# Optimization experiments

Measured on AMD Instinct MI355X. Metric: run time of the kernel, lower is better.

## Reference

```python
import jax, jax.numpy as jnp
import numpy as np

D_MODEL = 2048
NUM_HEADS = 16
D_K = D_MODEL // NUM_HEADS
ROPE_THETA = 10000.0
B, S = 2, 2048


def setup_inputs() -> dict:
    key = jax.random.key(0)
    ks = jax.random.split(key, 5)
    std = 1.0 / np.sqrt(D_MODEL)
    return {
        "x": jax.random.normal(ks[0], (B, S, D_MODEL), jnp.float32),
        "wq": jax.random.normal(ks[1], (D_MODEL, D_MODEL), jnp.float32) * std,
        "wk": jax.random.normal(ks[2], (D_MODEL, D_MODEL), jnp.float32) * std,
        "wv": jax.random.normal(ks[3], (D_MODEL, D_MODEL), jnp.float32) * std,
        "wo": jax.random.normal(ks[4], (D_MODEL, D_MODEL), jnp.float32) * std,
        "token_positions": jnp.arange(S, dtype=jnp.int32),
    }


def _rope(x, positions):
    # x: [b, h, s, d_k]; positions: [s]
    inv_freq = 1.0 / (ROPE_THETA ** (jnp.arange(0, D_K, 2, dtype=jnp.float32) / D_K))
    freqs = positions.astype(jnp.float32)[:, None] * inv_freq[None, :]  # [s, d_k/2]
    cos, sin = jnp.cos(freqs), jnp.sin(freqs)
    x_even, x_odd = x[..., ::2], x[..., 1::2]
    out_even = x_even * cos - x_odd * sin
    out_odd = x_even * sin + x_odd * cos
    # re-interleave even/odd lanes
    return jnp.stack([out_even, out_odd], axis=-1).reshape(x.shape)


def reference(x, wq, wk, wv, wo, token_positions):
    b, s, _ = x.shape
    # projections: weight is [out, in] as in torch Linear-style einsum
    q = jnp.einsum("bsd,ed->bse", x, wq)
    k = jnp.einsum("bsd,ed->bse", x, wk)
    v = jnp.einsum("bsd,ed->bse", x, wv)
    # split heads: b s (h d) -> b h s d
    def split(t):
        return t.reshape(b, s, NUM_HEADS, D_K).transpose(0, 2, 1, 3)
    q, k, v = split(q), split(k), split(v)
    q = _rope(q, token_positions)
    k = _rope(k, token_positions)
    scores = jnp.einsum("bhmd,bhnd->bhmn", q, k) / jnp.sqrt(jnp.float32(D_K))
    causal = jnp.tril(jnp.ones((s, s), dtype=bool))
    scores = jnp.where(causal[None, None], scores, -jnp.inf)
    attn = jax.nn.softmax(scores, axis=-1)
    out = jnp.einsum("bhmn,bhnd->bhmd", attn, v)
    out = out.transpose(0, 2, 1, 3).reshape(b, s, D_MODEL)
    return jnp.einsum("em,bsm->bse", wo, out)
```

## Files before the change

### kernel.cpp

```cpp
#include <hip/hip_runtime.h>

#define S_LEN 2048
#define DM 2048
#define NH 16
#define DK 128
#define BB 2
#define BH (BB*NH)
#define GK 2048

typedef float f32x4 __attribute__((ext_vector_type(4)));
typedef __bf16 bf16x8 __attribute__((ext_vector_type(8)));
typedef unsigned int u32;

#define AS1 __attribute__((address_space(1)))
#define AS3 __attribute__((address_space(3)))

__device__ inline void gload16(const void* g, void* l){
  __builtin_amdgcn_global_load_lds((AS1 const u32*)g, (AS3 u32*)l, 16, 0, 0);
}

__device__ inline ushort f2bf(float f){
  unsigned u = __float_as_uint(f);
  u = (u + 0x7FFFu + ((u >> 16) & 1u)) >> 16;
  return (ushort)u;
}

__global__ void k_f32_to_bf16(const float* __restrict__ in, ushort* __restrict__ out, int n4){
  int i = blockIdx.x * blockDim.x + threadIdx.x;
  if (i >= n4) return;
  float4 v = reinterpret_cast<const float4*>(in)[i];
  ushort4 o;
  o.x = f2bf(v.x); o.y = f2bf(v.y); o.z = f2bf(v.z); o.w = f2bf(v.w);
  reinterpret_cast<ushort4*>(out)[i] = o;
}

__global__ void k_w4(const float* __restrict__ wq, const float* __restrict__ wk,
                     const float* __restrict__ wv, const float* __restrict__ wo4,
                     ushort* __restrict__ dqkv, ushort* __restrict__ dwo){
  int i = blockIdx.x * 256 + threadIdx.x;
  int sel = i >> 20;
  int off = i & ((1 << 20) - 1);
  const float* s = (sel == 0) ? wq : (sel == 1) ? wk : (sel == 2) ? wv : wo4;
  ushort* d = (sel < 3) ? (dqkv + (size_t)sel * DM * DM) : dwo;
  float4 v = reinterpret_cast<const float4*>(s)[off];
  ushort4 o;
  o.x = f2bf(v.x); o.y = f2bf(v.y); o.z = f2bf(v.z); o.w = f2bf(v.w);
  reinterpret_cast<ushort4*>(d)[off] = o;
}

__global__ void k_rope_table(const int* __restrict__ pos, float2* __restrict__ cs){
  int idx = blockIdx.x * 256 + threadIdx.x;
  if (idx >= S_LEN * 64) return;
  int s = idx >> 6, i = idx & 63;
  float inv = expf(-0.14391156831212787f * (float)i);
  float f = (float)pos[s] * inv;
  cs[idx] = make_float2(cosf(f), sinf(f));
}

#define SBAR() do{ __builtin_amdgcn_s_barrier(); __builtin_amdgcn_sched_barrier(0); }while(0)
#define VMC(n) asm volatile("s_waitcnt vmcnt(" #n ")" ::: "memory")

#define STG(slot, srcp, tks, khh) do{ \
  const ushort* _s = (srcp) + (tks)*64 + (khh)*32; \
  gload16(_s,                    lds + (slot)*8192 + wid*512); \
  gload16(_s + (size_t)128*GK,   lds + (slot)*8192 + 4096 + wid*512); \
}while(0)

#define RD_A(slot, mh) do{ \
  af[0] = *reinterpret_cast<const bf16x8*>(ldsc + (slot)*16384 + wm*8192 + ((mh)*4+0)*1024 + frA); \
  af[1] = *reinterpret_cast<const bf16x8*>(ldsc + (slot)*16384 + wm*8192 + ((mh)*4+1)*1024 + frA); \
  af[2] = *reinterpret_cast<const bf16x8*>(ldsc + (slot)*16384 + wm*8192 + ((mh)*4+2)*1024 + frA); \
  af[3] = *reinterpret_cast<const bf16x8*>(ldsc + (slot)*16384 + wm*8192 + ((mh)*4+3)*1024 + frA); \
}while(0)

#define RD_B(slot) do{ \
  bfr[0] = *reinterpret_cast<const bf16x8*>(ldsc + (slot)*16384 + wn*4096 + 0*1024 + frA); \
  bfr[1] = *reinterpret_cast<const bf16x8*>(ldsc + (slot)*16384 + wn*4096 + 1*1024 + frA); \
  bfr[2] = *reinterpret_cast<const bf16x8*>(ldsc + (slot)*16384 + wn*4096 + 2*1024 + frA); \
  bfr[3] = *reinterpret_cast<const bf16x8*>(ldsc + (slot)*16384 + wn*4096 + 3*1024 + frA); \
}while(0)

#define MM(mh) do{ \
  __builtin_amdgcn_s_setprio(1); \
  _Pragma("unroll") \
  for (int mf2 = 0; mf2 < 4; mf2++) \
    _Pragma("unroll") \
    for (int nf = 0; nf < 4; nf++) \
      acc[(mh)*4+mf2][nf] = __builtin_amdgcn_mfma_f32_16x16x32_bf16(af[mf2], bfr[nf], acc[(mh)*4+mf2][nf], 0, 0, 0); \
  __builtin_amdgcn_s_setprio(0); \
}while(0)

__launch_bounds__(512, 2)
__global__ void k_gemm_qk(const ushort* __restrict__ A, const ushort* __restrict__ Bt,
                          const float2* __restrict__ cs,
                          ushort* __restrict__ Qh, ushort* __restrict__ Kh){
  __shared__ short lds[65536];
  const int tid = threadIdx.x, lane = tid & 63, wid = tid >> 6;
  const int wm = wid >> 2, wn = wid & 3;
  const int fr = lane & 15, fq = lane >> 4;

  const int bid = blockIdx.x;
  const int b2 = (bid & 7) * 32 + (bid >> 3);
  const int by = b2 >> 4, bx = b2 & 15;

  const int rbase = wid * 16 + (lane >> 2);
  const int kup = ((lane & 3) ^ ((lane >> 3) & 3)) * 8;
  const ushort* pa = A  + (size_t)(by * 256 + rbase) * GK + kup;
  const ushort* pb = Bt + (size_t)(bx * 256 + rbase) * GK + kup;

  const char* ldsc = (const char*)lds;
  const int frA = fr * 64 + ((fq * 16) ^ (((fr >> 1) & 3) << 4));

  f32x4 acc[8][4] = {};
  bf16x8 af[4], bfr[4];

  STG(0, pa, 0, 0); STG(1, pb, 0, 0); STG(2, pa, 0, 1); STG(3, pb, 0, 1);
  STG(4, pa, 1, 0); STG(5, pb, 1, 0);
  VMC(8);
  SBAR();

  #pragma unroll 1
  for (int it = 0; it < 16; ++it){
    const int tb  = 2 * it + 1;
    const int tn  = (2 * it + 2 < 32) ? 2 * it + 2 : 31;
    const int tn1 = (2 * it + 3 < 32) ? 2 * it + 3 : 31;
    RD_A(0, 0); RD_B(1); STG(6, pa, tb, 1);           SBAR(); MM(0); SBAR();
    RD_A(0, 1);          STG(7, pb, tb, 1);  VMC(6);  SBAR(); MM(1); SBAR();
    RD_A(2, 0); RD_B(3); STG(0, pa, tn, 0);           SBAR(); MM(0); SBAR();
    RD_A(2, 1);          STG(1, pb, tn, 0);  VMC(6);  SBAR(); MM(1); SBAR();
    RD_A(4, 0); RD_B(5); STG(2, pa, tn, 1);           SBAR(); MM(0); SBAR();
    RD_A(4, 1);          STG(3, pb, tn, 1);  VMC(6);  SBAR(); MM(1); SBAR();
    RD_A(6, 0); RD_B(7); STG(4, pa, tn1, 0);          SBAR(); MM(0); SBAR();
    RD_A(6, 1);          STG(5, pb, tn1, 0); VMC(6);  SBAR(); MM(1); SBAR();
  }

  const int rowb = by * 256 + wm * 128 + fq * 4;
  ushort* dst = (bx < 8) ? Qh : Kh;
  #pragma unroll
  for (int mf = 0; mf < 8; mf++)
    #pragma unroll
    for (int nf = 0; nf < 4; nf++){
      int col = bx * 256 + wn * 64 + nf * 16 + fr;
      int cg = col & 2047;
      int hh = cg >> 7, dd = cg & 127, jj = (cg >> 1) & 63;
      #pragma unroll
      for (int i = 0; i < 4; i++){
        int row = rowb + mf * 16 + i;
        int s = row & (S_LEN - 1), bb = row >> 11;
        float2 c2 = cs[s * 64 + jj];
        float v = acc[mf][nf][i];
        float p = __shfl_xor(v, 1);
        float o = (fr & 1) ? fmaf(p, c2.y, v * c2.x) : fmaf(v, c2.x, -p * c2.y);
        dst[((size_t)(bb * NH + hh) * S_LEN + s) * DK + dd] = f2bf(o);
      }
    }
}

#define WSTG_A(si, tks, khh) do{ \
  const ushort* _s = pa + (tks)*64 + (khh)*32; \
  gload16(_s,                  lds + (si)*8192 + wid*512); \
  gload16(_s + (size_t)128*GK, lds + (si)*8192 + 4096 + wid*512); \
}while(0)
#define WSTG_B(si, tks, khh) do{ \
  const ushort* _s = pb + (tks)*64 + (khh)*32; \
  gload16(_s, lds + 32768 + (si)*4096 + wid*512); \
}while(0)
#define WRD_A(si, mhf) do{ \
  af[0] = *reinterpret_cast<const bf16x8*>(ldsc + (si)*16384 + wm*4096 + ((mhf)*2+0)*1024 + frA); \
  af[1] = *reinterpret_cast<const bf16x8*>(ldsc + (si)*16384 + wm*4096 + ((mhf)*2+1)*1024 + frA); \
}while(0)
#define WRD_B(si) do{ \
  bfr[0] = *reinterpret_cast<const bf16x8*>(ldsc + 65536 + (si)*8192 + wn*4096 + 0*1024 + frA); \
  bfr[1] = *reinterpret_cast<const bf16x8*>(ldsc + 65536 + (si)*8192 + wn*4096 + 1*1024 + frA); \
  bfr[2] = *reinterpret_cast<const bf16x8*>(ldsc + 65536 + (si)*8192 + wn*4096 + 2*1024 + frA); \
  bfr[3] = *reinterpret_cast<const bf16x8*>(ldsc + 65536 + (si)*8192 + wn*4096 + 3*1024 + frA); \
}while(0)
#define WMM(mhf) do{ \
  __builtin_amdgcn_s_setprio(1); \
  _Pragma("unroll") \
  for (int k2 = 0; k2 < 2; k2++) \
    _Pragma("unroll") \
    for (int nf = 0; nf < 4; nf++) \
      acc[(mhf)*2+k2][nf] = __builtin_amdgcn_mfma_f32_16x16x32_bf16(af[k2], bfr[nf], acc[(mhf)*2+k2][nf], 0, 0, 0); \
  __builtin_amdgcn_s_setprio(0); \
}while(0)

#define WBODY() \
  WSTG_A(0, 0, 0); WSTG_B(0, 0, 0); WSTG_A(1, 0, 1); WSTG_B(1, 0, 1); \
  WSTG_A(2, 1, 0); WSTG_B(2, 1, 0); \
  VMC(6); \
  SBAR(); \
  _Pragma("unroll 1") \
  for (int it = 0; it < 16; ++it){ \
    const int tb  = 2 * it + 1; \
    const int tn  = (2 * it + 2 < 32) ? 2 * it + 2 : 31; \
    const int tn1 = (2 * it + 3 < 32) ? 2 * it + 3 : 31; \
    WRD_A(0, 0); WRD_B(0); WSTG_A(3, tb, 1);            SBAR(); WMM(0); SBAR(); \
    WRD_A(0, 1);           WSTG_B(3, tb, 1);  VMC(6);   SBAR(); WMM(1); SBAR(); \
    WRD_A(1, 0); WRD_B(1); WSTG_A(0, tn, 0);            SBAR(); WMM(0); SBAR(); \
    WRD_A(1, 1);           WSTG_B(0, tn, 0);  VMC(6);   SBAR(); WMM(1); SBAR(); \
    WRD_A(2, 0); WRD_B(2); WSTG_A(1, tn, 1);            SBAR(); WMM(0); SBAR(); \
    WRD_A(2, 1);           WSTG_B(1, tn, 1);  VMC(6);   SBAR(); WMM(1); SBAR(); \
    WRD_A(3, 0); WRD_B(3); WSTG_A(2, tn1, 0);           SBAR(); WMM(0); SBAR(); \
    WRD_A(3, 1);           WSTG_B(2, tn1, 0); VMC(6);   SBAR(); WMM(1); SBAR(); \
  }

__launch_bounds__(512, 2)
__global__ void k_gemm_v(const ushort* __restrict__ A, const ushort* __restrict__ Bt,
                         ushort* __restrict__ Vt){
  __shared__ short lds[49152];
  const int tid = threadIdx.x, lane = tid & 63, wid = tid >> 6;
  const int wm = wid >> 1, wn = wid & 1;
  const int fr = lane & 15, fq = lane >> 4;

  const int bid = blockIdx.x;
  const int b2 = (bid & 7) * 32 + (bid >> 3);
  const int by = b2 >> 4, bx = b2 & 15;

  const int rbase = wid * 16 + (lane >> 2);
  const int kup = ((lane & 3) ^ ((lane >> 3) & 3)) * 8;
  const ushort* pa = A  + (size_t)(by * 256 + rbase) * GK + kup;
  const ushort* pb = Bt + (size_t)(bx * 128 + rbase) * GK + kup;

  const char* ldsc = (const char*)lds;
  const int frA = fr * 64 + ((fq * 16) ^ (((fr >> 1) & 3) << 4));

  f32x4 acc[4][4] = {};
  bf16x8 af[2], bfr[4];

  WBODY();

  const int rowb = by * 256 + wm * 64 + fq * 4;
  #pragma unroll
  for (int mf = 0; mf < 4; mf++){
    int row0 = rowb + mf * 16;
    int s0 = row0 & (S_LEN - 1), bb = row0 >> 11;
    #pragma unroll
    for (int nf = 0; nf < 4; nf++){
      int col = bx * 128 + wn * 64 + nf * 16 + fr;
      int hh = col >> 7, dd = col & 127;
      ushort4 o;
      o.x = f2bf(acc[mf][nf][0]); o.y = f2bf(acc[mf][nf][1]);
      o.z = f2bf(acc[mf][nf][2]); o.w = f2bf(acc[mf][nf][3]);
      *reinterpret_cast<ushort4*>(&Vt[((size_t)(bb * NH + hh) * DK + dd) * S_LEN + s0]) = o;
    }
  }
}

__launch_bounds__(512, 2)
__global__ void k_gemm_wo(const ushort* __restrict__ A, const ushort* __restrict__ Bt,
                          float* __restrict__ C){
  __shared__ short lds[49152];
  const int tid = threadIdx.x, lane = tid & 63, wid = tid >> 6;
  const int wm = wid >> 1, wn = wid & 1;
  const int fr = lane & 15, fq = lane >> 4;

  const int bid = blockIdx.x;
  const int b2 = (bid & 7) * 32 + (bid >> 3);
  const int by = b2 >> 4, bx = b2 & 15;

  const int rbase = wid * 16 + (lane >> 2);
  const int kup = ((lane & 3) ^ ((lane >> 3) & 3)) * 8;
  const ushort* pa = A  + (size_t)(by * 256 + rbase) * GK + kup;
  const ushort* pb = Bt + (size_t)(bx * 128 + rbase) * GK + kup;

  const char* ldsc = (const char*)lds;
  const int frA = fr * 64 + ((fq * 16) ^ (((fr >> 1) & 3) << 4));

  f32x4 acc[4][4] = {};
  bf16x8 af[2], bfr[4];

  WBODY();

  const int orow = by * 256 + wm * 64 + fq * 4;
  const int ocol = bx * 128 + wn * 64 + fr;
  #pragma unroll
  for (int mf = 0; mf < 4; mf++)
    #pragma unroll
    for (int nf = 0; nf < 4; nf++)
      #pragma unroll
      for (int i = 0; i < 4; i++)
        C[(size_t)(orow + mf * 16 + i) * DM + ocol + nf * 16] = acc[mf][nf][i];
}

__launch_bounds__(512)
__global__ void k_attn(const ushort* __restrict__ Q, const ushort* __restrict__ K,
                       const ushort* __restrict__ Vt, ushort* __restrict__ O){
  __shared__ short Kt[2][64 * 128];
  __shared__ short Vl[2][128 * 64];
  __shared__ short Pl[8][16 * 64];
  const int tid = threadIdx.x, lane = tid & 63, wid = tid >> 6;
  const int bid = blockIdx.x;
  const int pid = bid >> 5;
  const int bh = bid & 31;
  const int b = bh >> 4, h = bh & 15;
  const int fr = lane & 15, fq = lane >> 4;
  const int swz = (fr & 7) << 4;

  const ushort* kb = K  + (size_t)bh * S_LEN * DK;
  const ushort* vb = Vt + (size_t)bh * DK * S_LEN;
  char* PlB = (char*)Pl + wid * 2048;
  const float scale = 0.08838834764831845f;
  ushort* ob = O + (size_t)b * S_LEN * DM;

  int kro[2], kco[2], vro[2], vco[2];
  #pragma unroll
  for (int jj = 0; jj < 2; jj++){
    int ins = wid * 2 + jj;
    kro[jj] = ins * 4 + (lane >> 4);
    kco[jj] = 8 * ((lane & 15) ^ (kro[jj] & 7));
    vro[jj] = ins * 8 + (lane >> 3);
    vco[jj] = 8 * ((lane & 7) ^ (vro[jj] & 7));
  }

  #pragma unroll 1
  for (int half = 0; half < 2; half++){
    const int j = half ? pid : 15 - pid;
    const int qr = j * 128 + wid * 16;
    const int nt = 2 * j + 2;

    bf16x8 qf[4];
    #pragma unroll
    for (int c = 0; c < 4; c++)
      qf[c] = *reinterpret_cast<const bf16x8*>(
          Q + ((size_t)bh * S_LEN + qr + fr) * DK + c * 32 + fq * 8);

    float mi[4], li[4];
    #pragma unroll
    for (int i = 0; i < 4; i++){ mi[i] = -1e30f; li[i] = 0.f; }
    f32x4 accO[8] = {};

    __syncthreads();
    #pragma unroll
    for (int jj = 0; jj < 2; jj++){
      int ins = wid * 2 + jj;
      gload16(kb + (size_t)kro[jj] * DK + kco[jj],      (char*)Kt + ins * 1024);
      gload16(vb + (size_t)vro[jj] * S_LEN + vco[jj],   (char*)Vl + ins * 1024);
    }
    __syncthreads();

    #pragma unroll 1
    for (int kt = 0; kt < nt; kt++){
      const int k0 = kt * 64;
      const int cur = kt & 1;
      if (kt + 1 < nt){
        const int k1 = k0 + 64;
        #pragma unroll
        for (int jj = 0; jj < 2; jj++){
          int ins = wid * 2 + jj;
          gload16(kb + (size_t)(k1 + kro[jj]) * DK + kco[jj],  (char*)Kt + (cur ^ 1) * 16384 + ins * 1024);
          gload16(vb + (size_t)vro[jj] * S_LEN + k1 + vco[jj], (char*)Vl + (cur ^ 1) * 16384 + ins * 1024);
        }
      }
      const char* KtB = (const char*)Kt + cur * 16384;
      const char* VlB = (const char*)Vl + cur * 16384;

      f32x4 sc[4] = {};
      #pragma unroll
      for (int c = 0; c < 4; c++){
        bf16x8 kf[4];
        #pragma unroll
        for (int ch = 0; ch < 4; ch++)
          kf[ch] = *reinterpret_cast<const bf16x8*>(
              KtB + (ch * 16 + fr) * 256 + ((c * 64 + fq * 16) ^ swz));
        #pragma unroll
        for (int ch = 0; ch < 4; ch++)
          sc[ch] = __builtin_amdgcn_mfma_f32_16x16x32_bf16(qf[c], kf[ch], sc[ch], 0, 0, 0);
      }

      const bool needmask = (k0 + 63 > qr);
      #pragma unroll
      for (int ch = 0; ch < 4; ch++)
        #pragma unroll
        for (int i = 0; i < 4; i++){
          float v = sc[ch][i] * scale;
          if (needmask && (k0 + ch * 16 + fr > qr + fq * 4 + i)) v = -1e30f;
          sc[ch][i] = v;
        }
      f32x4 mx;
      #pragma unroll
      for (int i = 0; i < 4; i++)
        mx[i] = fmaxf(fmaxf(sc[0][i], sc[1][i]), fmaxf(sc[2][i], sc[3][i]));
      #pragma unroll
      for (int off = 1; off < 16; off <<= 1)
        #pragma unroll
        for (int i = 0; i < 4; i++) mx[i] = fmaxf(mx[i], __shfl_xor(mx[i], off));
      float scl[4];
      #pragma unroll
      for (int i = 0; i < 4; i++){
        float mn = fmaxf(mi[i], mx[i]);
        scl[i] = __expf(mi[i] - mn);
        mi[i] = mn;
      }
      #pragma unroll
      for (int ch = 0; ch < 4; ch++)
        #pragma unroll
        for (int i = 0; i < 4; i++) sc[ch][i] = __expf(sc[ch][i] - mi[i]);
      f32x4 rs;
      #pragma unroll
      for (int i = 0; i < 4; i++)
        rs[i] = (sc[0][i] + sc[1][i]) + (sc[2][i] + sc[3][i]);
      #pragma unroll
      for (int off = 1; off < 16; off <<= 1)
        #pragma unroll
        for (int i = 0; i < 4; i++) rs[i] += __shfl_xor(rs[i], off);
      #pragma unroll
      for (int i = 0; i < 4; i++) li[i] = li[i] * scl[i] + rs[i];
      #pragma unroll
      for (int dt = 0; dt < 8; dt++)
        #pragma unroll
        for (int i = 0; i < 4; i++) accO[dt][i] *= scl[i];

      #pragma unroll
      for (int ch = 0; ch < 4; ch++)
        #pragma unroll
        for (int i = 0; i < 4; i++){
          int q = fq * 4 + i;
          int off = q * 128 + ((ch * 32 + fr * 2) ^ ((q & 7) << 4));
          *reinterpret_cast<short*>(PlB + off) = (short)f2bf(sc[ch][i]);
        }
      bf16x8 pf[2];
      #pragma unroll
      for (int c2 = 0; c2 < 2; c2++)
        pf[c2] = *reinterpret_cast<const bf16x8*>(
            PlB + fr * 128 + ((c2 * 64 + fq * 16) ^ swz));

      #pragma unroll
      for (int dt = 0; dt < 8; dt++)
        #pragma unroll
        for (int c2 = 0; c2 < 2; c2++){
          bf16x8 vf = *reinterpret_cast<const bf16x8*>(
              VlB + (dt * 16 + fr) * 128 + ((c2 * 64 + fq * 16) ^ swz));
          accO[dt] = __builtin_amdgcn_mfma_f32_16x16x32_bf16(pf[c2], vf, accO[dt], 0, 0, 0);
        }
      __syncthreads();
    }

    float inv[4];
    #pragma unroll
    for (int i = 0; i < 4; i++) inv[i] = 1.f / li[i];
    #pragma unroll
    for (int dt = 0; dt < 8; dt++)
      #pragma unroll
      for (int i = 0; i < 4; i++){
        int row = qr + fq * 4 + i;
        ob[(size_t)row * DM + h * DK + dt * 16 + fr] = f2bf(accO[dt][i] * inv[i]);
      }
  }
}

extern "C" void kernel_launch(void* const* d_in, const int* in_sizes, int n_in,
                              void* d_out, int out_size, void* d_ws, size_t ws_size,
                              hipStream_t stream){
  const float* x  = (const float*)d_in[0];
  const float* wq = (const float*)d_in[1];
  const float* wk = (const float*)d_in[2];
  const float* wv = (const float*)d_in[3];
  const float* wo = (const float*)d_in[4];
  const int* pos  = (const int*)d_in[5];
  float* out = (float*)d_out;

  char* ws = (char*)d_ws;
  ushort* xb   = (ushort*)(ws);
  ushort* Ob   = xb;
  ushort* wqkv = (ushort*)(ws + 16777216);
  ushort* Qh   = (ushort*)(ws + 41943040);
  ushort* Kh   = (ushort*)(ws + 58720256);
  ushort* Vt   = (ushort*)(ws + 75497472);
  float2* cs   = (float2*)(ws + 92274688);
  ushort* wob  = (ushort*)(ws + 93323264);

  const int M = BB * S_LEN;

  k_rope_table<<<(S_LEN * 64) / 256, 256, 0, stream>>>(pos, cs);
  k_f32_to_bf16<<<(M * DM / 4) / 256, 256, 0, stream>>>(x, xb, M * DM / 4);
  k_w4<<<4 * (DM * DM / 4) / 256, 256, 0, stream>>>(wq, wk, wv, wo, wqkv, wob);

  k_gemm_qk<<<256, 512, 0, stream>>>(xb, wqkv, cs, Qh, Kh);
  k_gemm_v<<<256, 512, 0, stream>>>(xb, wqkv + (size_t)2 * DM * DM, Vt);

  k_attn<<<256, 512, 0, stream>>>(Qh, Kh, Vt, Ob);

  k_gemm_wo<<<256, 512, 0, stream>>>(Ob, wob, out);
}
```

Before: 282.3 us.

## Have each attention wave process 32 query rows to reuse K/V fragments

The attention kernel drops from 8 waves to 4 waves per block, and each wave now handles two 16-row query sub-tiles. K and V fragments read from LDS are reused across both sub-tiles, which halves LDS read traffic per MFMA. Each thread issues twice as many async global-to-LDS loads, and the P staging buffer is resized with a padded 160-byte row stride. The cost is higher register pressure (two sets of accumulators and softmax state per wave) and fewer waves per block to hide latency.

```diff
diff --git a/kernel.cpp b/kernel.cpp
--- a/kernel.cpp
+++ b/kernel.cpp
@@ -283,12 +283,12 @@
         C[(size_t)(orow + mf * 16 + i) * DM + ocol + nf * 16] = acc[mf][nf][i];
 }
 
-__launch_bounds__(512)
+__launch_bounds__(256)
 __global__ void k_attn(const ushort* __restrict__ Q, const ushort* __restrict__ K,
                        const ushort* __restrict__ Vt, ushort* __restrict__ O){
   __shared__ short Kt[2][64 * 128];
   __shared__ short Vl[2][128 * 64];
-  __shared__ short Pl[8][16 * 64];
+  __shared__ short Pl[4][32 * 80];
   const int tid = threadIdx.x, lane = tid & 63, wid = tid >> 6;
   const int bid = blockIdx.x;
   const int pid = bid >> 5;
@@ -299,14 +299,14 @@
 
   const ushort* kb = K  + (size_t)bh * S_LEN * DK;
   const ushort* vb = Vt + (size_t)bh * DK * S_LEN;
-  char* PlB = (char*)Pl + wid * 2048;
+  char* PlB = (char*)Pl + wid * 5120;
   const float scale = 0.08838834764831845f;
   ushort* ob = O + (size_t)b * S_LEN * DM;
 
-  int kro[2], kco[2], vro[2], vco[2];
+  int kro[4], kco[4], vro[4], vco[4];
   #pragma unroll
-  for (int jj = 0; jj < 2; jj++){
-    int ins = wid * 2 + jj;
+  for (int jj = 0; jj < 4; jj++){
+    int ins = wid * 4 + jj;
     kro[jj] = ins * 4 + (lane >> 4);
     kco[jj] = 8 * ((lane & 15) ^ (kro[jj] & 7));
     vro[jj] = ins * 8 + (lane >> 3);
@@ -316,26 +316,33 @@
   #pragma unroll 1
   for (int half = 0; half < 2; half++){
     const int j = half ? pid : 15 - pid;
-    const int qr = j * 128 + wid * 16;
+    const int qr = j * 128 + wid * 32;
     const int nt = 2 * j + 2;
 
-    bf16x8 qf[4];
+    bf16x8 qf[2][4];
     #pragma unroll
-    for (int c = 0; c < 4; c++)
-      qf[c] = *reinterpret_cast<const bf16x8*>(
-          Q + ((size_t)bh * S_LEN + qr + fr) * DK + c * 32 + fq * 8);
-
-    float mi[4], li[4];
+    for (int m = 0; m < 2; m++)
+      #pragma unroll
+      for (int c = 0; c < 4; c++)
+        qf[m][c] = *reinterpret_cast<const bf16x8*>(
+            Q + ((size_t)bh * S_LEN + qr + m * 16 + fr) * DK + c * 32 + fq * 8);
+
+    float mi[2][4], li[2][4];
     #pragma unroll
-    for (int i = 0; i < 4; i++){ mi[i] = -1e30f; li[i] = 0.f; }
-    f32x4 accO[8] = {};
+    for (int m = 0; m < 2; m++)
+      #pragma unroll
+      for (int i = 0; i < 4; i++){ mi[m][i] = -1e30f; li[m][i] = 0.f; }
+    f32x4 accO[2][8] = {};
 
     __syncthreads();
-    #pragma unroll
-    for (int jj = 0; jj < 2; jj++){
-      int ins = wid * 2 + jj;
-      gload16(kb + (size_t)kro[jj] * DK + kco[jj],      (char*)Kt + ins * 1024);
-      gload16(vb + (size_t)vro[jj] * S_LEN + vco[jj],   (char*)Vl + ins * 1024);
+    {
+      char* kd = (char*)Kt + (wid * 4) * 1024;
+      char* vd = (char*)Vl + (wid * 4) * 1024;
+      #pragma unroll
+      for (int jj = 0; jj < 4; jj++){
+        gload16(kb + (size_t)kro[jj] * DK + kco[jj],      kd + jj * 1024);
+        gload16(vb + (size_t)vro[jj] * S_LEN + vco[jj],   vd + jj * 1024);
+      }
     }
     __syncthreads();
 
@@ -345,17 +352,18 @@
       const int cur = kt & 1;
       if (kt + 1 < nt){
         const int k1 = k0 + 64;
-        #pragma unroll
-        for (int jj = 0; jj < 2; jj++){
-          int ins = wid * 2 + jj;
-          gload16(kb + (size_t)(k1 + kro[jj]) * DK + kco[jj],  (char*)Kt + (cur ^ 1) * 16384 + ins * 1024);
-          gload16(vb + (size_t)vro[jj] * S_LEN + k1 + vco[jj], (char*)Vl + (cur ^ 1) * 16384 + ins * 1024);
+        char* kd = (char*)Kt + (cur ^ 1) * 16384 + (wid * 4) * 1024;
+        char* vd = (char*)Vl + (cur ^ 1) * 16384 + (wid * 4) * 1024;
+        #pragma unroll
+        for (int jj = 0; jj < 4; jj++){
+          gload16(kb + (size_t)(k1 + kro[jj]) * DK + kco[jj],    kd + jj * 1024);
+          gload16(vb + (size_t)vro[jj] * S_LEN + k1 + vco[jj],   vd + jj * 1024);
         }
       }
       const char* KtB = (const char*)Kt + cur * 16384;
       const char* VlB = (const char*)Vl + cur * 16384;
 
-      f32x4 sc[4] = {};
+      f32x4 sc[2][4] = {};
       #pragma unroll
       for (int c = 0; c < 4; c++){
         bf16x8 kf[4];
@@ -364,66 +372,75 @@
           kf[ch] = *reinterpret_cast<const bf16x8*>(
               KtB + (ch * 16 + fr) * 256 + ((c * 64 + fq * 16) ^ swz));
         #pragma unroll
+        for (int ch = 0; ch < 4; ch++){
+          sc[0][ch] = __builtin_amdgcn_mfma_f32_16x16x32_bf16(qf[0][c], kf[ch], sc[0][ch], 0, 0, 0);
+          sc[1][ch] = __builtin_amdgcn_mfma_f32_16x16x32_bf16(qf[1][c], kf[ch], sc[1][ch], 0, 0, 0);
+        }
+      }
+
+      #pragma unroll
+      for (int m = 0; m < 2; m++){
+        const int qb = qr + m * 16;
+        const bool needmask = (k0 + 63 > qb);
+        #pragma unroll
         for (int ch = 0; ch < 4; ch++)
-          sc[ch] = __builtin_amdgcn_mfma_f32_16x16x32_bf16(qf[c], kf[ch], sc[ch], 0, 0, 0);
+          #pragma unroll
+          for (int i = 0; i < 4; i++){
+            float v = sc[m][ch][i] * scale;
+            if (needmask && (k0 + ch * 16 + fr > qb + fq * 4 + i)) v = -1e30f;
+            sc[m][ch][i] = v;
+          }
+        f32x4 mx;
+        #pragma unroll
+        for (int i = 0; i < 4; i++)
+          mx[i] = fmaxf(fmaxf(sc[m][0][i], sc[m][1][i]), fmaxf(sc[m][2][i], sc[m][3][i]));
+        #pragma unroll
+        for (int off = 1; off < 16; off <<= 1)
+          #pragma unroll
+          for (int i = 0; i < 4; i++) mx[i] = fmaxf(mx[i], __shfl_xor(mx[i], off));
+        float scl[4];
+        #pragma unroll
+        for (int i = 0; i < 4; i++){
+          float mn = fmaxf(mi[m][i], mx[i]);
+          scl[i] = __expf(mi[m][i] - mn);
+          mi[m][i] = mn;
+        }
+        #pragma unroll
+        for (int ch = 0; ch < 4; ch++)
+          #pragma unroll
+          for (int i = 0; i < 4; i++) sc[m][ch][i] = __expf(sc[m][ch][i] - mi[m][i]);
+        f32x4 rs;
+        #pragma unroll
+        for (int i = 0; i < 4; i++)
+          rs[i] = (sc[m][0][i] + sc[m][1][i]) + (sc[m][2][i] + sc[m][3][i]);
+        #pragma unroll
+        for (int off = 1; off < 16; off <<= 1)
+          #pragma unroll
+          for (int i = 0; i < 4; i++) rs[i] += __shfl_xor(rs[i], off);
+        #pragma unroll
+        for (int i = 0; i < 4; i++) li[m][i] = li[m][i] * scl[i] + rs[i];
+        #pragma unroll
+        for (int dt = 0; dt < 8; dt++)
+          #pragma unroll
+          for (int i = 0; i < 4; i++) accO[m][dt][i] *= scl[i];
+
+        #pragma unroll
+        for (int ch = 0; ch < 4; ch++)
+          #pragma unroll
+          for (int i = 0; i < 4; i++){
+            int q = m * 16 + fq * 4 + i;
+            int off = q * 160 + ((ch * 32 + fr * 2) ^ ((q & 7) << 4));
+            *reinterpret_cast<short*>(PlB + off) = (short)f2bf(sc[m][ch][i]);
+          }
       }
 
-      const bool needmask = (k0 + 63 > qr);
-      #pragma unroll
-      for (int ch = 0; ch < 4; ch++)
-        #pragma unroll
-        for (int i = 0; i < 4; i++){
-          float v = sc[ch][i] * scale;
-          if (needmask && (k0 + ch * 16 + fr > qr + fq * 4 + i)) v = -1e30f;
-          sc[ch][i] = v;
-        }
-      f32x4 mx;
-      #pragma unroll
-      for (int i = 0; i < 4; i++)
-        mx[i] = fmaxf(fmaxf(sc[0][i], sc[1][i]), fmaxf(sc[2][i], sc[3][i]));
-      #pragma unroll
-      for (int off = 1; off < 16; off <<= 1)
-        #pragma unroll
-        for (int i = 0; i < 4; i++) mx[i] = fmaxf(mx[i], __shfl_xor(mx[i], off));
-      float scl[4];
-      #pragma unroll
-      for (int i = 0; i < 4; i++){
-        float mn = fmaxf(mi[i], mx[i]);
-        scl[i] = __expf(mi[i] - mn);
-        mi[i] = mn;
-      }
-      #pragma unroll
-      for (int ch = 0; ch < 4; ch++)
-        #pragma unroll
-        for (int i = 0; i < 4; i++) sc[ch][i] = __expf(sc[ch][i] - mi[i]);
-      f32x4 rs;
-      #pragma unroll
-      for (int i = 0; i < 4; i++)
-        rs[i] = (sc[0][i] + sc[1][i]) + (sc[2][i] + sc[3][i]);
-      #pragma unroll
-      for (int off = 1; off < 16; off <<= 1)
-        #pragma unroll
-        for (int i = 0; i < 4; i++) rs[i] += __shfl_xor(rs[i], off);
-      #pragma unroll
-      for (int i = 0; i < 4; i++) li[i] = li[i] * scl[i] + rs[i];
-      #pragma unroll
-      for (int dt = 0; dt < 8; dt++)
-        #pragma unroll
-        for (int i = 0; i < 4; i++) accO[dt][i] *= scl[i];
-
-      #pragma unroll
-      for (int ch = 0; ch < 4; ch++)
-        #pragma unroll
-        for (int i = 0; i < 4; i++){
-          int q = fq * 4 + i;
-          int off = q * 128 + ((ch * 32 + fr * 2) ^ ((q & 7) << 4));
-          *reinterpret_cast<short*>(PlB + off) = (short)f2bf(sc[ch][i]);
-        }
-      bf16x8 pf[2];
-      #pragma unroll
-      for (int c2 = 0; c2 < 2; c2++)
-        pf[c2] = *reinterpret_cast<const bf16x8*>(
-            PlB + fr * 128 + ((c2 * 64 + fq * 16) ^ swz));
+      bf16x8 pf[2][2];
+      #pragma unroll
+      for (int m = 0; m < 2; m++)
+        #pragma unroll
+        for (int c2 = 0; c2 < 2; c2++)
+          pf[m][c2] = *reinterpret_cast<const bf16x8*>(
+              PlB + (m * 16 + fr) * 160 + ((c2 * 64 + fq * 16) ^ swz));
 
       #pragma unroll
       for (int dt = 0; dt < 8; dt++)
@@ -431,21 +448,25 @@
         for (int c2 = 0; c2 < 2; c2++){
           bf16x8 vf = *reinterpret_cast<const bf16x8*>(
               VlB + (dt * 16 + fr) * 128 + ((c2 * 64 + fq * 16) ^ swz));
-          accO[dt] = __builtin_amdgcn_mfma_f32_16x16x32_bf16(pf[c2], vf, accO[dt], 0, 0, 0);
+          accO[0][dt] = __builtin_amdgcn_mfma_f32_16x16x32_bf16(pf[0][c2], vf, accO[0][dt], 0, 0, 0);
+          accO[1][dt] = __builtin_amdgcn_mfma_f32_16x16x32_bf16(pf[1][c2], vf, accO[1][dt], 0, 0, 0);
         }
       __syncthreads();
     }
 
-    float inv[4];
     #pragma unroll
-    for (int i = 0; i < 4; i++) inv[i] = 1.f / li[i];
-    #pragma unroll
-    for (int dt = 0; dt < 8; dt++)
-      #pragma unroll
-      for (int i = 0; i < 4; i++){
-        int row = qr + fq * 4 + i;
-        ob[(size_t)row * DM + h * DK + dt * 16 + fr] = f2bf(accO[dt][i] * inv[i]);
-      }
+    for (int m = 0; m < 2; m++){
+      float inv[4];
+      #pragma unroll
+      for (int i = 0; i < 4; i++) inv[i] = 1.f / li[m][i];
+      #pragma unroll
+      for (int dt = 0; dt < 8; dt++)
+        #pragma unroll
+        for (int i = 0; i < 4; i++){
+          int row = qr + m * 16 + fq * 4 + i;
+          ob[(size_t)row * DM + h * DK + dt * 16 + fr] = f2bf(accO[m][dt][i] * inv[i]);
+        }
+    }
   }
 }
 
@@ -479,7 +500,7 @@
   k_gemm_qk<<<256, 512, 0, stream>>>(xb, wqkv, cs, Qh, Kh);
   k_gemm_v<<<256, 512, 0, stream>>>(xb, wqkv + (size_t)2 * DM * DM, Vt);
 
-  k_attn<<<256, 512, 0, stream>>>(Qh, Kh, Vt, Ob);
+  k_attn<<<256, 256, 0, stream>>>(Qh, Kh, Vt, Ob);
 
   k_gemm_wo<<<256, 512, 0, stream>>>(Ob, wob, out);
 }
```

After: 319.5 us. +13.2%, slower.

## Transpose QK^T MFMA so each lane owns one query row for softmax

Applied to the files above, without the earlier changes.

Swaps the MFMA operands in the score computation so the score tile is transposed and each lane holds a full query row's values in its registers. Row max and sum then need only two cross-lane shuffles instead of four per value set, and the online-softmax state shrinks to one scalar per lane. P is written to LDS as packed 8-byte stores into a padded (160-byte stride) buffer instead of scattered 2-byte swizzled stores. The accumulator rescale and final normalisation now need extra shuffles to redistribute per-row scale factors, and LDS use grows slightly.

```diff
diff --git a/kernel.cpp b/kernel.cpp
--- a/kernel.cpp
+++ b/kernel.cpp
@@ -288,7 +288,7 @@
                        const ushort* __restrict__ Vt, ushort* __restrict__ O){
   __shared__ short Kt[2][64 * 128];
   __shared__ short Vl[2][128 * 64];
-  __shared__ short Pl[8][16 * 64];
+  __shared__ short Pl[8][16 * 80];
   const int tid = threadIdx.x, lane = tid & 63, wid = tid >> 6;
   const int bid = blockIdx.x;
   const int pid = bid >> 5;
@@ -299,7 +299,7 @@
 
   const ushort* kb = K  + (size_t)bh * S_LEN * DK;
   const ushort* vb = Vt + (size_t)bh * DK * S_LEN;
-  char* PlB = (char*)Pl + wid * 2048;
+  char* PlB = (char*)Pl + wid * 2560;
   const float scale = 0.08838834764831845f;
   ushort* ob = O + (size_t)b * S_LEN * DM;
 
@@ -325,9 +325,7 @@
       qf[c] = *reinterpret_cast<const bf16x8*>(
           Q + ((size_t)bh * S_LEN + qr + fr) * DK + c * 32 + fq * 8);
 
-    float mi[4], li[4];
-    #pragma unroll
-    for (int i = 0; i < 4; i++){ mi[i] = -1e30f; li[i] = 0.f; }
+    float mi = -1e30f, li = 0.f;
     f32x4 accO[8] = {};
 
     __syncthreads();
@@ -365,65 +363,64 @@
               KtB + (ch * 16 + fr) * 256 + ((c * 64 + fq * 16) ^ swz));
         #pragma unroll
         for (int ch = 0; ch < 4; ch++)
-          sc[ch] = __builtin_amdgcn_mfma_f32_16x16x32_bf16(qf[c], kf[ch], sc[ch], 0, 0, 0);
+          sc[ch] = __builtin_amdgcn_mfma_f32_16x16x32_bf16(kf[ch], qf[c], sc[ch], 0, 0, 0);
       }
 
       const bool needmask = (k0 + 63 > qr);
+      const int qrow = qr + fr;
       #pragma unroll
       for (int ch = 0; ch < 4; ch++)
         #pragma unroll
         for (int i = 0; i < 4; i++){
           float v = sc[ch][i] * scale;
-          if (needmask && (k0 + ch * 16 + fr > qr + fq * 4 + i)) v = -1e30f;
+          if (needmask && (k0 + ch * 16 + fq * 4 + i > qrow)) v = -1e30f;
           sc[ch][i] = v;
         }
-      f32x4 mx;
-      #pragma unroll
-      for (int i = 0; i < 4; i++)
-        mx[i] = fmaxf(fmaxf(sc[0][i], sc[1][i]), fmaxf(sc[2][i], sc[3][i]));
-      #pragma unroll
-      for (int off = 1; off < 16; off <<= 1)
-        #pragma unroll
-        for (int i = 0; i < 4; i++) mx[i] = fmaxf(mx[i], __shfl_xor(mx[i], off));
-      float scl[4];
-      #pragma unroll
-      for (int i = 0; i < 4; i++){
-        float mn = fmaxf(mi[i], mx[i]);
-        scl[i] = __expf(mi[i] - mn);
-        mi[i] = mn;
+
+      float mx = sc[0][0];
+      #pragma unroll
+      for (int ch = 0; ch < 4; ch++)
+        #pragma unroll
+        for (int i = 0; i < 4; i++) mx = fmaxf(mx, sc[ch][i]);
+      mx = fmaxf(mx, __shfl_xor(mx, 16));
+      mx = fmaxf(mx, __shfl_xor(mx, 32));
+
+      float mn = fmaxf(mi, mx);
+      float scl = __expf(mi - mn);
+      mi = mn;
+
+      float rs = 0.f;
+      #pragma unroll
+      for (int ch = 0; ch < 4; ch++)
+        #pragma unroll
+        for (int i = 0; i < 4; i++){
+          float e = __expf(sc[ch][i] - mn);
+          sc[ch][i] = e;
+          rs += e;
+        }
+      rs += __shfl_xor(rs, 16);
+      rs += __shfl_xor(rs, 32);
+      li = li * scl + rs;
+
+      float sclq[4];
+      #pragma unroll
+      for (int i = 0; i < 4; i++) sclq[i] = __shfl(scl, fq * 4 + i);
+      #pragma unroll
+      for (int dt = 0; dt < 8; dt++)
+        #pragma unroll
+        for (int i = 0; i < 4; i++) accO[dt][i] *= sclq[i];
+
+      #pragma unroll
+      for (int ch = 0; ch < 4; ch++){
+        uint2 pk;
+        pk.x = (u32)f2bf(sc[ch][0]) | ((u32)f2bf(sc[ch][1]) << 16);
+        pk.y = (u32)f2bf(sc[ch][2]) | ((u32)f2bf(sc[ch][3]) << 16);
+        *reinterpret_cast<uint2*>(PlB + fr * 160 + ch * 32 + fq * 8) = pk;
       }
-      #pragma unroll
-      for (int ch = 0; ch < 4; ch++)
-        #pragma unroll
-        for (int i = 0; i < 4; i++) sc[ch][i] = __expf(sc[ch][i] - mi[i]);
-      f32x4 rs;
-      #pragma unroll
-      for (int i = 0; i < 4; i++)
-        rs[i] = (sc[0][i] + sc[1][i]) + (sc[2][i] + sc[3][i]);
-      #pragma unroll
-      for (int off = 1; off < 16; off <<= 1)
-        #pragma unroll
-        for (int i = 0; i < 4; i++) rs[i] += __shfl_xor(rs[i], off);
-      #pragma unroll
-      for (int i = 0; i < 4; i++) li[i] = li[i] * scl[i] + rs[i];
-      #pragma unroll
-      for (int dt = 0; dt < 8; dt++)
-        #pragma unroll
-        for (int i = 0; i < 4; i++) accO[dt][i] *= scl[i];
-
-      #pragma unroll
-      for (int ch = 0; ch < 4; ch++)
-        #pragma unroll
-        for (int i = 0; i < 4; i++){
-          int q = fq * 4 + i;
-          int off = q * 128 + ((ch * 32 + fr * 2) ^ ((q & 7) << 4));
-          *reinterpret_cast<short*>(PlB + off) = (short)f2bf(sc[ch][i]);
-        }
       bf16x8 pf[2];
       #pragma unroll
       for (int c2 = 0; c2 < 2; c2++)
-        pf[c2] = *reinterpret_cast<const bf16x8*>(
-            PlB + fr * 128 + ((c2 * 64 + fq * 16) ^ swz));
+        pf[c2] = *reinterpret_cast<const bf16x8*>(PlB + fr * 160 + c2 * 64 + fq * 16);
 
       #pragma unroll
       for (int dt = 0; dt < 8; dt++)
@@ -438,7 +435,7 @@
 
     float inv[4];
     #pragma unroll
-    for (int i = 0; i < 4; i++) inv[i] = 1.f / li[i];
+    for (int i = 0; i < 4; i++) inv[i] = 1.f / __shfl(li, fq * 4 + i);
     #pragma unroll
     for (int dt = 0; dt < 8; dt++)
       #pragma unroll
```

New measurement: 261.4 us. 7.4% less time.
